# Performance work log

Measured on AMD Instinct MI355X. Metric: run time of the kernel, lower is better.

Reference implementation:

```python
import jax, jax.numpy as jnp
import numpy as np

NEG_SLOPE = 0.2
EPS = 1e-16


def setup_inputs() -> dict:
    N, E, IN, H, C = 100000, 1600000, 128, 4, 16
    key = jax.random.key(0)
    k1, k2, k3, k4, k5 = jax.random.split(key, 5)
    x = jax.random.normal(k1, (N, IN), dtype=jnp.float32)
    edge_index = jax.random.randint(k2, (2, E), 0, N, dtype=jnp.int64)
    # Xavier-uniform init like nn.init.xavier_uniform_
    limW = float(np.sqrt(6.0 / (IN + H * C)))
    W = jax.random.uniform(k3, (IN, H * C), dtype=jnp.float32, minval=-limW, maxval=limW)
    lima = float(np.sqrt(6.0 / (H + C)))
    att = jax.random.uniform(k4, (1, H, C), dtype=jnp.float32, minval=-lima, maxval=lima)
    bias = jnp.zeros((H * C,), dtype=jnp.float32)
    return {"x": x, "edge_index": edge_index, "W": W, "att": att, "bias": bias}


def reference(x, edge_index, W, att, bias):
    N = x.shape[0]
    H, C = att.shape[1], att.shape[2]
    h = (x @ W).reshape(N, H, C)  # [N,H,C]
    # add self loops
    loops = jnp.arange(N, dtype=edge_index.dtype)
    row = jnp.concatenate([edge_index[0], loops])  # target nodes
    col = jnp.concatenate([edge_index[1], loops])  # source nodes
    x_i = h[row]  # [Etot,H,C]
    x_j = h[col]
    e = jax.nn.leaky_relu(x_i + x_j, NEG_SLOPE)
    alpha = jnp.einsum('ehc,hc->eh', e, att[0])  # [Etot,H]
    # segment softmax keyed by row (every node has a self loop -> no empty segments)
    amax = jax.lax.stop_gradient(jax.ops.segment_max(alpha, row, num_segments=N))
    ea = jnp.exp(alpha - amax[row])
    denom = jax.ops.segment_sum(ea, row, num_segments=N)
    alpha = ea / (denom[row] + EPS)
    # weighted message scatter-add (dropout p=0 / eval mode)
    out = jax.ops.segment_sum(x_j * alpha[:, :, None], row, num_segments=N)  # [N,H,C]
    out = out.reshape(N, H * C) + bias  # concat=True
    return out
```

## Files before the change

### kernel.cpp

```cpp
#include <hip/hip_runtime.h>

#define NEG_SLOPE 0.2f

typedef float f32x4 __attribute__((ext_vector_type(4)));
typedef short bf16x8 __attribute__((ext_vector_type(8)));

__device__ __forceinline__ unsigned short f2bf(float f) {
  union { float f; unsigned u; } v; v.f = f;
  unsigned r = v.u + 0x7fff + ((v.u >> 16) & 1);
  return (unsigned short)(r >> 16);
}
__device__ __forceinline__ unsigned pkbf(float a, float b) {
  return (unsigned)f2bf(a) | ((unsigned)f2bf(b) << 16);
}
__device__ __forceinline__ f32x4 upk4(unsigned ux, unsigned uy) {
  union { unsigned u; float f; } a, b, c, d;
  a.u = ux << 16; b.u = ux & 0xffff0000u;
  c.u = uy << 16; d.u = uy & 0xffff0000u;
  f32x4 r; r.x = a.f; r.y = b.f; r.z = c.f; r.w = d.f;
  return r;
}
__device__ __forceinline__ f32x4 absfma(f32x4 s, f32x4 coef, f32x4 d) {
  d.x = fmaf(fabsf(s.x), coef.x, d.x);
  d.y = fmaf(fabsf(s.y), coef.y, d.y);
  d.z = fmaf(fabsf(s.z), coef.z, d.z);
  d.w = fmaf(fabsf(s.w), coef.w, d.w);
  return d;
}
__device__ __forceinline__ float dpp_xor1_add(float x) {
  int y = __builtin_amdgcn_mov_dpp(__builtin_bit_cast(int, x), 0xB1, 0xF, 0xF, true);
  return x + __builtin_bit_cast(float, y);
}
__device__ __forceinline__ float dpp_xor2_add(float x) {
  int y = __builtin_amdgcn_mov_dpp(__builtin_bit_cast(int, x), 0x4E, 0xF, 0xF, true);
  return x + __builtin_bit_cast(float, y);
}

#define TILE 4096
#define EPT 16
#define NBKT_MAX 256
#define SMEM_BYTES 24576

__device__ __forceinline__ void gemm_role(const float* __restrict__ x,
                                          const float* __restrict__ W,
                                          unsigned short* __restrict__ hb, int N,
                                          char* smem, int bid) {
  uint4* Bl = (uint4*)smem;
  const int t = threadIdx.x;
  {
    const int l = t & 63;
    const int kt = (t >> 6) & 3;
    const int kb = kt * 32 + ((l >> 4) * 8);
    const int cb = l & 15;
#pragma unroll
    for (int ct = 0; ct < 4; ct++) {
      const float* wp = W + (size_t)kb * 64 + ct * 16 + cb;
      unsigned p[4];
#pragma unroll
      for (int jj = 0; jj < 4; jj++)
        p[jj] = pkbf(wp[(2 * jj) * 64], wp[(2 * jj + 1) * 64]);
      Bl[(ct * 4 + kt) * 64 + l] = make_uint4(p[0], p[1], p[2], p[3]);
    }
  }
  __syncthreads();
  const int l = t & 63;
  const int wv = t >> 6;
  union BU { bf16x8 v; uint4 q; };
  BU b[4][4];
#pragma unroll
  for (int ct = 0; ct < 4; ct++)
#pragma unroll
    for (int kt = 0; kt < 4; kt++) b[ct][kt].q = Bl[(ct * 4 + kt) * 64 + l];

  const int rowbase0 = bid * 256 + wv * 64;
#pragma unroll
  for (int rt = 0; rt < 4; rt++) {
    const int rbase = rowbase0 + rt * 16;
    int rl = rbase + (l & 15);
    if (rl >= N) rl = N - 1;
    const float* xp = x + (size_t)rl * 128 + ((l >> 4) * 8);
    BU ah[4];
#pragma unroll
    for (int kt = 0; kt < 4; kt++) {
      float4 v0 = *(const float4*)(xp + kt * 32);
      float4 v1 = *(const float4*)(xp + kt * 32 + 4);
      ah[kt].q = make_uint4(pkbf(v0.x, v0.y), pkbf(v0.z, v0.w),
                            pkbf(v1.x, v1.y), pkbf(v1.z, v1.w));
    }
#pragma unroll
    for (int ct = 0; ct < 4; ct++) {
      f32x4 acc = {0.f, 0.f, 0.f, 0.f};
#pragma unroll
      for (int kt = 0; kt < 4; kt++) {
        acc = __builtin_amdgcn_mfma_f32_16x16x32_bf16(ah[kt].v, b[ct][kt].v, acc, 0, 0, 0);
      }
#pragma unroll
      for (int j = 0; j < 4; j++) {
        float v = acc[j];
        float pv = __shfl_xor(v, 1);
        int row = rbase + (l >> 4) * 4 + j;
        if (!(l & 1) && row < N) {
          *(unsigned*)((char*)hb + (size_t)row * 128 + ct * 32 + (l & 15) * 2) =
              pkbf(v, pv);
        }
      }
    }
  }
}

__device__ __forceinline__ void bucket_role(const int* __restrict__ rowi,
                                            const int* __restrict__ coli,
                                            int* __restrict__ bucket_fill,
                                            unsigned* __restrict__ bucket_arr, int E,
                                            int Cedge, int Ctot, int NBKT, char* smem,
                                            int bid) {
  int* cnt = (int*)smem;
  int* gadj = cnt + 256;
  int* tmp = gadj + 256;
  unsigned* staged = (unsigned*)(tmp + 256);
  unsigned char* bkof = (unsigned char*)(staged + TILE);
  const int t = threadIdx.x;
  const int tile0 = bid * TILE;
  const int nt = min(TILE, E - tile0);
  cnt[t] = 0;
  __syncthreads();
  unsigned pk[EPT];
  int bk[EPT];
#pragma unroll
  for (int j = 0; j < EPT; j++) {
    int i = tile0 + j * 256 + t;
    if (i < E) {
      int r = rowi[i];
      int c = coli[i];
      bk[j] = r >> 9;
      pk[j] = ((unsigned)(r & 511) << 17) | (unsigned)c;
      atomicAdd(&cnt[bk[j]], 1);
    } else {
      bk[j] = -1;
    }
  }
  __syncthreads();
  int v = cnt[t];
  tmp[t] = v;
  __syncthreads();
  for (int off = 1; off < 256; off <<= 1) {
    int val = tmp[t] + ((t >= off) ? tmp[t - off] : 0);
    __syncthreads();
    tmp[t] = val;
    __syncthreads();
  }
  int ex = tmp[t] - v;
  int ga = 0;
  if (v > 0) ga = atomicAdd(&bucket_fill[t], v);
  gadj[t] = ga - ex;
  cnt[t] = ex;
  __syncthreads();
#pragma unroll
  for (int j = 0; j < EPT; j++) {
    if (bk[j] >= 0) {
      int lp = atomicAdd(&cnt[bk[j]], 1);
      staged[lp] = pk[j];
      bkof[lp] = (unsigned char)bk[j];
    }
  }
  __syncthreads();
  for (int i = t; i < nt; i += 256) {
    int b = bkof[i];
    int pb = i + gadj[b];
    if (pb < Cedge) bucket_arr[b * Ctot + pb] = staged[i];
  }
}

__global__ __launch_bounds__(256) void gemm_bucket(const float* __restrict__ x,
                                                   const float* __restrict__ W,
                                                   unsigned short* __restrict__ hb, int N,
                                                   const int* __restrict__ rowi,
                                                   const int* __restrict__ coli,
                                                   int* __restrict__ bucket_fill,
                                                   unsigned* __restrict__ bucket_arr,
                                                   int E, int Cedge, int Ctot, int NBKT,
                                                   int G1) {
  __shared__ __align__(16) char smem[SMEM_BYTES];
  if ((int)blockIdx.x < G1)
    gemm_role(x, W, hb, N, smem, blockIdx.x);
  else
    bucket_role(rowi, coli, bucket_fill, bucket_arr, E, Cedge, Ctot, NBKT, smem,
                blockIdx.x - G1);
}

#define STAGE_CAP 10240

__global__ __launch_bounds__(1024) void csr_pass(unsigned* __restrict__ bucket_arr,
                                                 const int* __restrict__ bucket_fill,
                                                 int2* __restrict__ rowinfo,
                                                 int Cedge, int Ctot, int N) {
  __shared__ unsigned stage[STAGE_CAP];
  __shared__ int hist[512], excl[512], pairs[256];
  const int t = threadIdx.x;
  const int b = blockIdx.x;
  const int bb = b * Ctot;
  const int r0 = b << 9;
  const int nb = min(bucket_fill[b], Cedge);
  for (int i = t; i < 512; i += 1024) hist[i] = ((r0 + i) < N) ? 1 : 0;
  for (int i = t; i < nb; i += 1024) stage[i] = bucket_arr[bb + i];
  __syncthreads();
  for (int i = t; i < nb; i += 1024) atomicAdd(&hist[stage[i] >> 17], 1);
  __syncthreads();
  int h0 = 0, h1 = 0, ps = 0;
  if (t < 256) {
    h0 = hist[2 * t];
    h1 = hist[2 * t + 1];
    ps = h0 + h1;
    pairs[t] = ps;
  }
  __syncthreads();
  for (int off = 1; off < 256; off <<= 1) {
    int val = 0;
    if (t < 256) val = pairs[t] + ((t >= off) ? pairs[t - off] : 0);
    __syncthreads();
    if (t < 256) pairs[t] = val;
    __syncthreads();
  }
  if (t < 256) {
    int pexcl = pairs[t] - ps;
    excl[2 * t] = pexcl;
    excl[2 * t + 1] = pexcl + h0;
  }
  __syncthreads();
  for (int r = t; r < 512; r += 1024) {
    int gr = r0 + r;
    if (gr < N) {
      int o = bb + excl[r];
      rowinfo[gr] = make_int2(o, o + hist[r]);
    }
  }
  __syncthreads();
  for (int i = t; i < nb; i += 1024) {
    unsigned pk = stage[i];
    int r = pk >> 17;
    int lp = atomicAdd(&excl[r], 1);
    bucket_arr[bb + lp] = (pk & 0x1FFFFu) << 7;
  }
  __syncthreads();
  for (int r = t; r < 512; r += 1024) {
    int gr = r0 + r;
    if (gr < N) bucket_arr[bb + excl[r]] = (unsigned)gr << 7;
  }
}

#define ESTEPN(hivX, accX, denX, u)                     \
  {                                                     \
    f32x4 jv = upk4((u).x, (u).y);                      \
    f32x4 s = hivX + jv;                                \
    f32x4 d = s * attA;                                 \
    d = absfma(s, attB, d);                             \
    float al = (d.x + d.y) + (d.z + d.w);               \
    al = dpp_xor1_add(al);                              \
    al = dpp_xor2_add(al);                              \
    float p = exp2f(al);                                \
    accX += jv * p;                                     \
    denX += p;                                          \
  }

__global__ __launch_bounds__(256) void node_pass(const unsigned short* __restrict__ hb,
                                                 const int2* __restrict__ rowinfo,
                                                 const unsigned* __restrict__ srcs,
                                                 const float* __restrict__ att,
                                                 const float* __restrict__ bias,
                                                 float* __restrict__ out, int N) {
  const int wp = (blockIdx.x * blockDim.x + threadIdx.x) >> 6;
  const int a = wp * 2;
  if (a >= N) return;
  const int bn = a + 1;
  const bool bval = bn < N;
  const int bc = bval ? bn : a;
  const int lane = threadIdx.x & 63;
  const int lr = lane & 15;
  const int q = lane >> 4;
  const char* hbc = (const char*)hb + (unsigned)(lr << 3);
  const unsigned* srcq = srcs + q;
  const f32x4 attv = *(const f32x4*)(att + 4 * lr);
  const f32x4 attA = attv * (0.6f * 1.44269504088896f);
  const f32x4 attB = attv * (0.4f * 1.44269504088896f);
  const int2 ria = rowinfo[a];
  const int2 rib = rowinfo[bc];
  uint2 hua = *(const uint2*)(hbc + ((size_t)a << 7));
  uint2 hub = *(const uint2*)(hbc + ((size_t)bc << 7));
  const f32x4 hivA = upk4(hua.x, hua.y);
  const f32x4 hivB = upk4(hub.x, hub.y);
  int ka = ria.x, kb = rib.x;
  const int ka1 = ria.y;
  const int kb1 = bval ? rib.y : rib.x;
  f32x4 accA = {0.f, 0.f, 0.f, 0.f};
  f32x4 accB = {0.f, 0.f, 0.f, 0.f};
  float denA = 0.f, denB = 0.f;
  while (ka + 8 <= ka1 && kb + 8 <= kb1) {
    uint2 ua0 = *(const uint2*)(hbc + srcq[ka]);
    uint2 ua1 = *(const uint2*)(hbc + srcq[ka + 4]);
    uint2 ub0 = *(const uint2*)(hbc + srcq[kb]);
    uint2 ub1 = *(const uint2*)(hbc + srcq[kb + 4]);
    ESTEPN(hivA, accA, denA, ua0);
    ESTEPN(hivA, accA, denA, ua1);
    ESTEPN(hivB, accB, denB, ub0);
    ESTEPN(hivB, accB, denB, ub1);
    ka += 8;
    kb += 8;
  }
  for (; ka + 8 <= ka1; ka += 8) {
    uint2 u0 = *(const uint2*)(hbc + srcq[ka]);
    uint2 u1 = *(const uint2*)(hbc + srcq[ka + 4]);
    ESTEPN(hivA, accA, denA, u0);
    ESTEPN(hivA, accA, denA, u1);
  }
  for (; kb + 8 <= kb1; kb += 8) {
    uint2 u0 = *(const uint2*)(hbc + srcq[kb]);
    uint2 u1 = *(const uint2*)(hbc + srcq[kb + 4]);
    ESTEPN(hivB, accB, denB, u0);
    ESTEPN(hivB, accB, denB, u1);
  }
  for (; ka + 4 <= ka1; ka += 4) {
    uint2 u = *(const uint2*)(hbc + srcq[ka]);
    ESTEPN(hivA, accA, denA, u);
  }
  for (; kb + 4 <= kb1; kb += 4) {
    uint2 u = *(const uint2*)(hbc + srcq[kb]);
    ESTEPN(hivB, accB, denB, u);
  }
  if (ka < ka1) {
    bool act = (ka + q) < ka1;
    uint2 u = *(const uint2*)(hbc + (act ? srcq[ka] : srcs[ka]));
    f32x4 jv = upk4(u.x, u.y);
    f32x4 s = hivA + jv;
    f32x4 d = s * attA;
    d = absfma(s, attB, d);
    float al = (d.x + d.y) + (d.z + d.w);
    al = dpp_xor1_add(al);
    al = dpp_xor2_add(al);
    float p = act ? exp2f(al) : 0.f;
    accA += jv * p;
    denA += p;
  }
  if (kb < kb1) {
    bool act = (kb + q) < kb1;
    uint2 u = *(const uint2*)(hbc + (act ? srcq[kb] : srcs[kb]));
    f32x4 jv = upk4(u.x, u.y);
    f32x4 s = hivB + jv;
    f32x4 d = s * attA;
    d = absfma(s, attB, d);
    float al = (d.x + d.y) + (d.z + d.w);
    al = dpp_xor1_add(al);
    al = dpp_xor2_add(al);
    float p = act ? exp2f(al) : 0.f;
    accB += jv * p;
    denB += p;
  }
#pragma unroll
  for (int j = 0; j < 4; j++) {
    accA[j] += __shfl_xor(accA[j], 16);
    accB[j] += __shfl_xor(accB[j], 16);
    accA[j] += __shfl_xor(accA[j], 32);
    accB[j] += __shfl_xor(accB[j], 32);
  }
  denA += __shfl_xor(denA, 16);
  denB += __shfl_xor(denB, 16);
  denA += __shfl_xor(denA, 32);
  denB += __shfl_xor(denB, 32);
  if (q == 0) {
    const f32x4 bv = *(const f32x4*)(bias + 4 * lr);
    float invA = 1.0f / (denA + 1e-16f);
    *(f32x4*)(out + (size_t)a * 64 + 4 * lr) = accA * invA + bv;
    if (bval) {
      float invB = 1.0f / (denB + 1e-16f);
      *(f32x4*)(out + (size_t)bn * 64 + 4 * lr) = accB * invB + bv;
    }
  }
}

extern "C" void kernel_launch(void* const* d_in, const int* in_sizes, int n_in,
                              void* d_out, int out_size, void* d_ws, size_t ws_size,
                              hipStream_t stream) {
  const float* x = (const float*)d_in[0];
  const int* eidx = (const int*)d_in[1];
  const float* W = (const float*)d_in[2];
  const float* att = (const float*)d_in[3];
  const float* bias = (const float*)d_in[4];
  float* out = (float*)d_out;

  const int N = in_sizes[0] / 128;
  const int E = in_sizes[1] / 2;
  const int NBKT = (N + 511) >> 9;
  int Cedge = (E + NBKT - 1) / NBKT;
  Cedge = Cedge + Cedge / 8 + 64;
  Cedge = (Cedge + 15) & ~15;
  if (Cedge > STAGE_CAP) Cedge = STAGE_CAP;
  const int Ctot = Cedge + 512;

  unsigned short* hb = (unsigned short*)d_ws;
  int* bucket_fill = (int*)(hb + (size_t)N * 64);
  int2* rowinfo = (int2*)(bucket_fill + NBKT_MAX);
  unsigned* bucket_arr = (unsigned*)(rowinfo + N);

  hipMemsetAsync(bucket_fill, 0, NBKT_MAX * sizeof(int), stream);

  const int G1 = (N + 255) / 256;
  const int G2 = (E + TILE - 1) / TILE;
  gemm_bucket<<<G1 + G2, 256, 0, stream>>>(x, W, hb, N, eidx, eidx + E, bucket_fill,
                                           bucket_arr, E, Cedge, Ctot, NBKT, G1);
  csr_pass<<<NBKT, 1024, 0, stream>>>(bucket_arr, bucket_fill, rowinfo, Cedge, Ctot, N);
  node_pass<<<(N * 32 + 255) / 256, 256, 0, stream>>>(hb, rowinfo, bucket_arr, att, bias,
                                                      out, N);
}
```

Baseline: 97.21 us.

## Use persistent work-queue blocks for fused GEMM and edge bucketing

Replaces the one-block-per-item launch of the GEMM and bucketing roles with 768 persistent blocks. Each block pulls work items from a global atomic counter, and the GEMM chunks are halved to 128 rows for finer balance. csr_pass also merges the bucket load loop with the histogram atomics, removing one pass over shared memory. The aim is to cut block launch and tail overhead, at the cost of a global atomic plus two barriers per item, and it reloads the W tile from global memory for every GEMM chunk.

```diff
diff --git a/kernel.cpp b/kernel.cpp
--- a/kernel.cpp
+++ b/kernel.cpp
@@ -40,11 +40,12 @@
 #define EPT 16
 #define NBKT_MAX 256
 #define SMEM_BYTES 24576
-
-__device__ __forceinline__ void gemm_role(const float* __restrict__ x,
-                                          const float* __restrict__ W,
-                                          unsigned short* __restrict__ hb, int N,
-                                          char* smem, int bid) {
+#define GCHUNK 128
+
+__device__ __forceinline__ void gemm_chunk(const float* __restrict__ x,
+                                           const float* __restrict__ W,
+                                           unsigned short* __restrict__ hb, int N,
+                                           char* smem, int bid) {
   uint4* Bl = (uint4*)smem;
   const int t = threadIdx.x;
   {
@@ -72,9 +73,9 @@
 #pragma unroll
     for (int kt = 0; kt < 4; kt++) b[ct][kt].q = Bl[(ct * 4 + kt) * 64 + l];
 
-  const int rowbase0 = bid * 256 + wv * 64;
-#pragma unroll
-  for (int rt = 0; rt < 4; rt++) {
+  const int rowbase0 = bid * GCHUNK + wv * 32;
+#pragma unroll
+  for (int rt = 0; rt < 2; rt++) {
     const int rbase = rowbase0 + rt * 16;
     int rl = rbase + (l & 15);
     if (rl >= N) rl = N - 1;
@@ -106,6 +107,7 @@
       }
     }
   }
+  __syncthreads();
 }
 
 __device__ __forceinline__ void bucket_role(const int* __restrict__ rowi,
@@ -169,23 +171,33 @@
     int pb = i + gadj[b];
     if (pb < Cedge) bucket_arr[b * Ctot + pb] = staged[i];
   }
-}
-
-__global__ __launch_bounds__(256) void gemm_bucket(const float* __restrict__ x,
-                                                   const float* __restrict__ W,
-                                                   unsigned short* __restrict__ hb, int N,
-                                                   const int* __restrict__ rowi,
-                                                   const int* __restrict__ coli,
-                                                   int* __restrict__ bucket_fill,
-                                                   unsigned* __restrict__ bucket_arr,
-                                                   int E, int Cedge, int Ctot, int NBKT,
-                                                   int G1) {
+  __syncthreads();
+}
+
+__global__ __launch_bounds__(256) void fused_k1(const float* __restrict__ x,
+                                                const float* __restrict__ W,
+                                                unsigned short* __restrict__ hb, int N,
+                                                const int* __restrict__ rowi,
+                                                const int* __restrict__ coli,
+                                                int* __restrict__ bucket_fill,
+                                                unsigned* __restrict__ bucket_arr,
+                                                int E, int Cedge, int Ctot, int NBKT,
+                                                int* __restrict__ wq, int NCG, int NCB) {
   __shared__ __align__(16) char smem[SMEM_BYTES];
-  if ((int)blockIdx.x < G1)
-    gemm_role(x, W, hb, N, smem, blockIdx.x);
-  else
-    bucket_role(rowi, coli, bucket_fill, bucket_arr, E, Cedge, Ctot, NBKT, smem,
-                blockIdx.x - G1);
+  __shared__ int wis;
+  const int total = NCG + NCB;
+  for (;;) {
+    if (threadIdx.x == 0) wis = atomicAdd(wq, 1);
+    __syncthreads();
+    const int wi = wis;
+    __syncthreads();
+    if (wi >= total) break;
+    if (wi < NCG)
+      gemm_chunk(x, W, hb, N, smem, wi);
+    else
+      bucket_role(rowi, coli, bucket_fill, bucket_arr, E, Cedge, Ctot, NBKT, smem,
+                  wi - NCG);
+  }
 }
 
 #define STAGE_CAP 10240
@@ -202,9 +214,12 @@
   const int r0 = b << 9;
   const int nb = min(bucket_fill[b], Cedge);
   for (int i = t; i < 512; i += 1024) hist[i] = ((r0 + i) < N) ? 1 : 0;
-  for (int i = t; i < nb; i += 1024) stage[i] = bucket_arr[bb + i];
-  __syncthreads();
-  for (int i = t; i < nb; i += 1024) atomicAdd(&hist[stage[i] >> 17], 1);
+  __syncthreads();
+  for (int i = t; i < nb; i += 1024) {
+    unsigned v = bucket_arr[bb + i];
+    stage[i] = v;
+    atomicAdd(&hist[v >> 17], 1);
+  }
   __syncthreads();
   int h0 = 0, h1 = 0, ps = 0;
   if (t < 256) {
@@ -397,15 +412,16 @@
 
   unsigned short* hb = (unsigned short*)d_ws;
   int* bucket_fill = (int*)(hb + (size_t)N * 64);
-  int2* rowinfo = (int2*)(bucket_fill + NBKT_MAX);
+  int* wq = bucket_fill + NBKT_MAX;
+  int2* rowinfo = (int2*)(wq + 16);
   unsigned* bucket_arr = (unsigned*)(rowinfo + N);
 
-  hipMemsetAsync(bucket_fill, 0, NBKT_MAX * sizeof(int), stream);
-
-  const int G1 = (N + 255) / 256;
-  const int G2 = (E + TILE - 1) / TILE;
-  gemm_bucket<<<G1 + G2, 256, 0, stream>>>(x, W, hb, N, eidx, eidx + E, bucket_fill,
-                                           bucket_arr, E, Cedge, Ctot, NBKT, G1);
+  hipMemsetAsync(bucket_fill, 0, (NBKT_MAX + 16) * sizeof(int), stream);
+
+  const int NCG = (N + GCHUNK - 1) / GCHUNK;
+  const int NCB = (E + TILE - 1) / TILE;
+  fused_k1<<<768, 256, 0, stream>>>(x, W, hb, N, eidx, eidx + E, bucket_fill, bucket_arr,
+                                    E, Cedge, Ctot, NBKT, wq, NCG, NCB);
   csr_pass<<<NBKT, 1024, 0, stream>>>(bucket_arr, bucket_fill, rowinfo, Cedge, Ctot, N);
   node_pass<<<(N * 32 + 255) / 256, 256, 0, stream>>>(hb, rowinfo, bucket_arr, att, bias,
                                                       out, N);
```

Result: slower. 110.4 us (+13.6%).
